# Performance work log

Measured on AMD Instinct MI355X. Metric: run time of the kernel, lower is better.

## Reference

```python
import jax, jax.numpy as jnp
import numpy as np

CAPACITY_FACTOR = 1.25


def setup_inputs() -> dict:
    key = jax.random.key(0)
    ks = jax.random.split(key, 5)
    B, N, D, E, H = 4, 2048, 1024, 8, 4096
    x = jax.random.normal(ks[0], (B, N, D), dtype=jnp.float32)
    w_router = jax.random.normal(ks[1], (D, E), dtype=jnp.float32) * 0.02
    w1 = jax.random.normal(ks[2], (E, D, H), dtype=jnp.float32) * 0.02
    b1 = jnp.zeros((E, H), dtype=jnp.float32)
    w2 = jax.random.normal(ks[3], (E, H, D), dtype=jnp.float32) * 0.02
    b2 = jnp.zeros((E, D), dtype=jnp.float32)
    return {"x": x, "w_router": w_router, "w1": w1, "b1": b1, "w2": w2, "b2": b2}


def reference(x, w_router, w1, b1, w2, b2):
    B, N, D = x.shape
    E = w_router.shape[1]
    C = int(N * CAPACITY_FACTOR // E)  # expert capacity

    # ---- top-1 switch router ----
    logits = jnp.einsum('bnd,de->bne', x, w_router)                 # [B,N,E]
    z = jax.nn.logsumexp(logits, axis=-1)                           # [B,N]
    router_z_loss = jnp.mean(z * z)
    probs = jax.nn.softmax(logits, axis=-1)                         # [B,N,E]
    gate = jnp.max(probs, axis=-1)                                  # [B,N]
    idx = jnp.argmax(probs, axis=-1)                                # [B,N]
    mask = jax.nn.one_hot(idx, E, dtype=x.dtype)                    # [B,N,E]

    # load-balancing aux loss (Switch-Transformer style)
    density = jnp.mean(mask, axis=1)                                # [B,E] fraction routed
    density_proxy = jnp.mean(probs, axis=1)                         # [B,E] mean router prob
    aux_loss = jnp.mean(jnp.sum(density * density_proxy, axis=-1)) * (E * E)

    # position within each expert; drop tokens beyond capacity
    pos = jnp.cumsum(mask, axis=1) - 1.0                            # [B,N,E]
    pos = pos.astype(jnp.int32)
    # one_hot zeros out indices outside [0,C); mask zeros unrouted slots
    dispatch = mask[..., None] * jax.nn.one_hot(pos, C, dtype=x.dtype)  # [B,N,E,C]
    combine = dispatch * gate[:, :, None, None]                     # [B,N,E,C]

    # ---- dense dispatch -> grouped expert FFN -> dense combine ----
    expert_inputs = jnp.einsum('bnd,bnec->becd', x, dispatch)       # [B,E,C,D]
    h = jax.nn.gelu(jnp.einsum('becd,edh->bech', expert_inputs, w1)
                    + b1[None, :, None, :])                          # [B,E,C,H]
    expert_outputs = jnp.einsum('bech,ehd->becd', h, w2) + b2[None, :, None, :]
    output = jnp.einsum('becd,bnec->bnd', expert_outputs, combine)  # [B,N,D]
    return output, aux_loss, router_z_loss
```

## Files before the change

### kernel.cpp

```cpp
#include <hip/hip_runtime.h>
#include <hip/hip_bf16.h>
#include <math.h>

#define B_ 4
#define N_ 2048
#define D_ 1024
#define E_ 8
#define H_ 4096
#define C_ 320
#define M_ (B_*C_)

typedef __attribute__((ext_vector_type(8))) short short8;
typedef __attribute__((ext_vector_type(4))) float floatx4;

__device__ __forceinline__ unsigned short f2bf(float f) {
  unsigned u = __builtin_bit_cast(unsigned, f);
  u += 0x7fffu + ((u >> 16) & 1u);
  return (unsigned short)(u >> 16);
}

__device__ __forceinline__ float gelu_fast(float x) {
  float u = 0.7978845608028654f * (x + 0.044715f * x * x * x);
  float t = 1.f - 2.f / (__expf(2.f * u) + 1.f);
  return 0.5f * x * (1.f + t);
}

__device__ __forceinline__ void gload_lds16(const unsigned short* g, unsigned short* l) {
  __builtin_amdgcn_global_load_lds(
      (const __attribute__((address_space(1))) unsigned int*)g,
      (__attribute__((address_space(3))) unsigned int*)l, 16, 0, 0);
}

__global__ __launch_bounds__(256) void router_kernel(
    const float* __restrict__ x, const float* __restrict__ wr,
    int* __restrict__ idx_buf, float* __restrict__ gate_buf,
    float* __restrict__ stats)
{
  int lane  = threadIdx.x & 63;
  int wave  = threadIdx.x >> 6;
  int token = blockIdx.x * 4 + wave;
  int b     = token >> 11;

  const float* xp = x + (size_t)token * D_ + lane * 16;
  float xv[16];
#pragma unroll
  for (int i = 0; i < 4; i++) {
    float4 v = ((const float4*)xp)[i];
    xv[i*4+0]=v.x; xv[i*4+1]=v.y; xv[i*4+2]=v.z; xv[i*4+3]=v.w;
  }
  double acc[8];
#pragma unroll
  for (int e = 0; e < 8; e++) acc[e] = 0.0;
  const float* wp = wr + (size_t)(lane * 16) * E_;
#pragma unroll
  for (int i = 0; i < 16; i++) {
    float xs = xv[i];
#pragma unroll
    for (int e = 0; e < 8; e++) acc[e] += (double)xs * (double)wp[i*8 + e];
  }
  for (int off = 32; off > 0; off >>= 1) {
#pragma unroll
    for (int e = 0; e < 8; e++) acc[e] += __shfl_xor(acc[e], off, 64);
  }

  float l[8];
#pragma unroll
  for (int e = 0; e < 8; e++) l[e] = (float)acc[e];
  float m = l[0]; int best = 0;
#pragma unroll
  for (int e = 1; e < 8; e++) if (l[e] > m) { m = l[e]; best = e; }
  float p[8], sum = 0.f;
#pragma unroll
  for (int e = 0; e < 8; e++) { p[e] = expf(l[e] - m); sum += p[e]; }
  float inv = 1.f / sum;
#pragma unroll
  for (int e = 0; e < 8; e++) p[e] *= inv;
  float z    = m + logf(sum);
  float gate = inv;

  __shared__ float s_cnt[8], s_prox[8], s_zsq[1];
  if (threadIdx.x < 8)  { s_cnt[threadIdx.x] = 0.f; s_prox[threadIdx.x] = 0.f; }
  if (threadIdx.x == 8) s_zsq[0] = 0.f;
  __syncthreads();
  if (lane == 0) {
    idx_buf[token]  = best;
    gate_buf[token] = gate;
    atomicAdd(&s_zsq[0], z * z);
    atomicAdd(&s_cnt[best], 1.f);
#pragma unroll
    for (int e = 0; e < 8; e++) atomicAdd(&s_prox[e], p[e]);
  }
  __syncthreads();
  if (threadIdx.x < 8) {
    atomicAdd(&stats[b*8 + threadIdx.x],      s_cnt[threadIdx.x]);
    atomicAdd(&stats[32 + b*8 + threadIdx.x], s_prox[threadIdx.x]);
  }
  if (threadIdx.x == 8) atomicAdd(&stats[64], s_zsq[0]);
}

__global__ __launch_bounds__(64) void pos_kernel(
    const int* __restrict__ idx_buf, int* __restrict__ slot_token,
    const float* __restrict__ stats, float* __restrict__ loss_out)
{
  int be = blockIdx.x;
  int b = be >> 3, e = be & 7;
  int lane = threadIdx.x;
  int base = 0;
  int* out = slot_token + (size_t)(e * B_ + b) * C_;
  for (int n0 = 0; n0 < N_; n0 += 64) {
    int n = n0 + lane;
    bool match = (idx_buf[b * N_ + n] == e);
    unsigned long long mask = __ballot(match);
    int my = base + __popcll(mask & ((1ull << lane) - 1ull));
    if (match && my < C_) out[my] = b * N_ + n;
    base += __popcll(mask);
  }
  if (be == 0 && lane == 0) {
    float aux = 0.f;
    for (int i = 0; i < 32; i++) aux += stats[i] * stats[32 + i];
    aux *= 64.f / ((float)B_ * (float)N_ * (float)N_);
    loss_out[0] = aux;
    loss_out[1] = stats[64] / (float)(B_ * N_);
  }
}

__global__ __launch_bounds__(256) void gather_kernel(
    const float* __restrict__ x, const int* __restrict__ slot_token,
    unsigned short* __restrict__ xe)
{
  int row = blockIdx.x;
  int t = slot_token[row];
  int col = threadIdx.x * 4;
  ushort4 o;
  if (t >= 0) {
    float4 v = *(const float4*)(x + (size_t)t * D_ + col);
    o.x = f2bf(v.x); o.y = f2bf(v.y); o.z = f2bf(v.z); o.w = f2bf(v.w);
  } else {
    o.x = 0; o.y = 0; o.z = 0; o.w = 0;
  }
  *(ushort4*)(xe + (size_t)row * D_ + col) = o;
}

__global__ __launch_bounds__(256) void transcast_kernel(
    const float* __restrict__ in, unsigned short* __restrict__ out, int R, int Cc)
{
  int e = blockIdx.z;
  const float* pin = in + (size_t)e * R * Cc;
  unsigned short* pout = out + (size_t)e * R * Cc;
  __shared__ float T[64][65];
  int r0 = blockIdx.y * 64, c0 = blockIdx.x * 64;
  {
    int row = threadIdx.x >> 2;
    int cb  = (threadIdx.x & 3) * 4;
#pragma unroll
    for (int p = 0; p < 4; p++) {
      int col = cb + p * 16;
      float4 v = *(const float4*)(pin + (size_t)(r0 + row) * Cc + c0 + col);
      T[row][col+0] = v.x; T[row][col+1] = v.y; T[row][col+2] = v.z; T[row][col+3] = v.w;
    }
  }
  __syncthreads();
  {
    int ocb = threadIdx.x >> 4;
    int or4 = (threadIdx.x & 15) * 4;
#pragma unroll
    for (int p = 0; p < 4; p++) {
      int oc = ocb + p * 16;
      ushort4 o;
      o.x = f2bf(T[or4+0][oc]); o.y = f2bf(T[or4+1][oc]);
      o.z = f2bf(T[or4+2][oc]); o.w = f2bf(T[or4+3][oc]);
      *(ushort4*)(pout + (size_t)(c0 + oc) * R + r0 + or4) = o;
    }
  }
}

template<int EPI>
__global__ __launch_bounds__(512, 2) void gemm_kernel(
    const unsigned short* __restrict__ A,
    const unsigned short* __restrict__ BT,
    const float* __restrict__ bias,
    unsigned short* __restrict__ Hout,
    float* __restrict__ Out,
    const int* __restrict__ slot_token,
    const float* __restrict__ gate_buf,
    int M, int K, int Nn, int MT)
{
  int e  = blockIdx.x & 7;
  int s  = blockIdx.x >> 3;
  int m0 = (s % MT) * 256;
  int n0 = (s / MT) * 256;
  const unsigned short* Ae = A  + (size_t)e * M  * K;
  const unsigned short* Be = BT + (size_t)e * Nn * K;

  __shared__ __align__(16) unsigned short As[2][256 * 64];
  __shared__ __align__(16) unsigned short Bs[2][256 * 64];
  __shared__ int   s_tok[256];
  __shared__ float s_gate[256];

  int tid  = threadIdx.x;
  int lane = tid & 63;
  int w    = tid >> 6;
  int wm   = (w >> 2) * 128;
  int wn   = (w & 3) * 64;
  int lr   = lane & 15;
  int quad = lane >> 4;
  int c0 = (((quad    ) ^ (lane & 7)) << 3);
  int c1 = (((quad + 4) ^ (lane & 7)) << 3);

  if constexpr (EPI == 1) {
    if (tid < 256) {
      int t = slot_token[(size_t)e * M + m0 + tid];
      s_tok[tid]  = t;
      s_gate[tid] = (t >= 0) ? gate_buf[t] : 0.f;
    }
  }

  floatx4 acc[8][4];
#pragma unroll
  for (int i = 0; i < 8; i++)
#pragma unroll
    for (int j = 0; j < 4; j++) acc[i][j] = (floatx4){0.f, 0.f, 0.f, 0.f};

  int rrow = lane >> 3;
  int sch  = ((lane & 7) ^ rrow) << 3;
  const unsigned short* gA00 = Ae + (size_t)(m0       + w*16     + rrow) * K + sch;
  const unsigned short* gA01 = Ae + (size_t)(m0       + w*16 + 8 + rrow) * K + sch;
  const unsigned short* gA10 = Ae + (size_t)(m0 + 128 + w*16     + rrow) * K + sch;
  const unsigned short* gA11 = Ae + (size_t)(m0 + 128 + w*16 + 8 + rrow) * K + sch;
  const unsigned short* gB00 = Be + (size_t)(n0       + w*16     + rrow) * K + sch;
  const unsigned short* gB01 = Be + (size_t)(n0       + w*16 + 8 + rrow) * K + sch;
  const unsigned short* gB10 = Be + (size_t)(n0 + 128 + w*16     + rrow) * K + sch;
  const unsigned short* gB11 = Be + (size_t)(n0 + 128 + w*16 + 8 + rrow) * K + sch;

#define STAGE_A(dbuf) do { \
    gload_lds16(gA00, &As[dbuf][(w*16    ) * 64]); \
    gload_lds16(gA01, &As[dbuf][(w*16 + 8) * 64]); \
    gload_lds16(gA10, &As[dbuf][(128 + w*16    ) * 64]); \
    gload_lds16(gA11, &As[dbuf][(128 + w*16 + 8) * 64]); \
    gA00 += 64; gA01 += 64; gA10 += 64; gA11 += 64; } while (0)
#define STAGE_B(dbuf) do { \
    gload_lds16(gB00, &Bs[dbuf][(w*16    ) * 64]); \
    gload_lds16(gB01, &Bs[dbuf][(w*16 + 8) * 64]); \
    gload_lds16(gB10, &Bs[dbuf][(128 + w*16    ) * 64]); \
    gload_lds16(gB11, &Bs[dbuf][(128 + w*16 + 8) * 64]); \
    gB00 += 64; gB01 += 64; gB10 += 64; gB11 += 64; } while (0)

  int nt = K >> 6;
  STAGE_A(0); STAGE_B(0);
  if (nt > 1) {
    STAGE_A(1); STAGE_B(1);
    asm volatile("s_waitcnt vmcnt(8)" ::: "memory");
  } else {
    asm volatile("s_waitcnt vmcnt(0)" ::: "memory");
  }
  __builtin_amdgcn_s_barrier();

  short8 af[4][2], bf[4][2];
  int cur = 0;
  for (int t = 0; t < nt; ++t) {
    int nxt = cur ^ 1;
    bool pf = (t + 2 < nt);
#pragma unroll
    for (int m = 0; m < 4; ++m) {
      int row = wm + m * 16 + lr;
      af[m][0] = *(const short8*)&As[cur][row * 64 + c0];
      af[m][1] = *(const short8*)&As[cur][row * 64 + c1];
    }
#pragma unroll
    for (int n = 0; n < 2; ++n) {
      int row = wn + n * 16 + lr;
      bf[n][0] = *(const short8*)&Bs[cur][row * 64 + c0];
      bf[n][1] = *(const short8*)&Bs[cur][row * 64 + c1];
    }
    __builtin_amdgcn_s_barrier();
    asm volatile("s_waitcnt lgkmcnt(0)" ::: "memory");
    __builtin_amdgcn_sched_barrier(0);
    __builtin_amdgcn_s_setprio(1);
#pragma unroll
    for (int m = 0; m < 4; ++m)
#pragma unroll
      for (int n = 0; n < 2; ++n) {
        acc[m][n] = __builtin_amdgcn_mfma_f32_16x16x32_bf16(af[m][0], bf[n][0], acc[m][n], 0, 0, 0);
        acc[m][n] = __builtin_amdgcn_mfma_f32_16x16x32_bf16(af[m][1], bf[n][1], acc[m][n], 0, 0, 0);
      }
    __builtin_amdgcn_s_setprio(0);
    __builtin_amdgcn_s_barrier();
#pragma unroll
    for (int n = 0; n < 2; ++n) {
      int row = wn + (n + 2) * 16 + lr;
      bf[n+2][0] = *(const short8*)&Bs[cur][row * 64 + c0];
      bf[n+2][1] = *(const short8*)&Bs[cur][row * 64 + c1];
    }
    __builtin_amdgcn_s_barrier();
    asm volatile("s_waitcnt lgkmcnt(0)" ::: "memory");
    __builtin_amdgcn_sched_barrier(0);
    __builtin_amdgcn_s_setprio(1);
#pragma unroll
    for (int m = 0; m < 4; ++m)
#pragma unroll
      for (int n = 2; n < 4; ++n) {
        acc[m][n] = __builtin_amdgcn_mfma_f32_16x16x32_bf16(af[m][0], bf[n][0], acc[m][n], 0, 0, 0);
        acc[m][n] = __builtin_amdgcn_mfma_f32_16x16x32_bf16(af[m][1], bf[n][1], acc[m][n], 0, 0, 0);
      }
    __builtin_amdgcn_s_setprio(0);
    __builtin_amdgcn_s_barrier();
#pragma unroll
    for (int m = 0; m < 4; ++m) {
      int row = wm + 64 + m * 16 + lr;
      af[m][0] = *(const short8*)&As[cur][row * 64 + c0];
      af[m][1] = *(const short8*)&As[cur][row * 64 + c1];
    }
    if (pf) STAGE_B(cur);
    __builtin_amdgcn_s_barrier();
    asm volatile("s_waitcnt lgkmcnt(0)" ::: "memory");
    __builtin_amdgcn_sched_barrier(0);
    __builtin_amdgcn_s_setprio(1);
#pragma unroll
    for (int m = 0; m < 4; ++m)
#pragma unroll
      for (int n = 2; n < 4; ++n) {
        acc[m+4][n] = __builtin_amdgcn_mfma_f32_16x16x32_bf16(af[m][0], bf[n][0], acc[m+4][n], 0, 0, 0);
        acc[m+4][n] = __builtin_amdgcn_mfma_f32_16x16x32_bf16(af[m][1], bf[n][1], acc[m+4][n], 0, 0, 0);
      }
    __builtin_amdgcn_s_setprio(0);
    __builtin_amdgcn_s_barrier();
    if (pf) STAGE_A(cur);
    __builtin_amdgcn_s_barrier();
    __builtin_amdgcn_s_setprio(1);
#pragma unroll
    for (int m = 0; m < 4; ++m)
#pragma unroll
      for (int n = 0; n < 2; ++n) {
        acc[m+4][n] = __builtin_amdgcn_mfma_f32_16x16x32_bf16(af[m][0], bf[n][0], acc[m+4][n], 0, 0, 0);
        acc[m+4][n] = __builtin_amdgcn_mfma_f32_16x16x32_bf16(af[m][1], bf[n][1], acc[m+4][n], 0, 0, 0);
      }
    __builtin_amdgcn_s_setprio(0);
    if (pf)                asm volatile("s_waitcnt vmcnt(8)" ::: "memory");
    else if (t + 1 < nt)   asm volatile("s_waitcnt vmcnt(0)" ::: "memory");
    __builtin_amdgcn_s_barrier();
    cur = nxt;
  }
#undef STAGE_A
#undef STAGE_B

#pragma unroll
  for (int m = 0; m < 8; ++m) {
    int rloc = wm + m * 16 + quad * 4;
#pragma unroll
    for (int n = 0; n < 4; ++n) {
      int col = n0 + wn + n * 16 + lr;
      float bz = bias[(size_t)e * Nn + col];
      if constexpr (EPI == 0) {
        size_t base = (size_t)e * M * Nn + (size_t)(m0 + rloc) * Nn + col;
#pragma unroll
        for (int r = 0; r < 4; r++)
          Hout[base + (size_t)r * Nn] = f2bf(gelu_fast(acc[m][n][r] + bz));
      } else {
#pragma unroll
        for (int r = 0; r < 4; r++) {
          int t = s_tok[rloc + r];
          if (t >= 0)
            Out[(size_t)t * D_ + col] = s_gate[rloc + r] * (acc[m][n][r] + bz);
        }
      }
    }
  }
}

extern "C" void kernel_launch(void* const* d_in, const int* in_sizes, int n_in,
                              void* d_out, int out_size, void* d_ws, size_t ws_size,
                              hipStream_t stream)
{
  (void)in_sizes; (void)n_in; (void)ws_size;
  const float* x  = (const float*)d_in[0];
  const float* wr = (const float*)d_in[1];
  const float* w1 = (const float*)d_in[2];
  const float* b1 = (const float*)d_in[3];
  const float* w2 = (const float*)d_in[4];
  const float* b2 = (const float*)d_in[5];
  float* out = (float*)d_out;

  char* ws = (char*)d_ws;
  int*   idx_buf  = (int*)(ws + 0);
  float* gate_buf = (float*)(ws + 32768);
  float* stats    = (float*)(ws + 65536);
  int*   slot_tok = (int*)(ws + 66560);
  unsigned short* xe  = (unsigned short*)(ws + 107520);
  unsigned short* wbf = (unsigned short*)(ws + 21079040);
  unsigned short* hbf = (unsigned short*)(ws + 88187904);

  hipMemsetAsync(d_out, 0, (size_t)out_size * 4, stream);
  hipMemsetAsync(stats, 0, 1024, stream);
  hipMemsetAsync(slot_tok, 0xFF, (size_t)E_ * B_ * C_ * 4, stream);

  router_kernel<<<(B_ * N_) / 4, 256, 0, stream>>>(x, wr, idx_buf, gate_buf, stats);
  pos_kernel<<<B_ * E_, 64, 0, stream>>>(idx_buf, slot_tok, stats,
                                         out + (size_t)B_ * N_ * D_);
  gather_kernel<<<E_ * M_, 256, 0, stream>>>(x, slot_tok, xe);

  transcast_kernel<<<dim3(H_ / 64, D_ / 64, E_), 256, 0, stream>>>(w1, wbf, D_, H_);
  gemm_kernel<0><<<E_ * (H_ / 256) * (M_ / 256), 512, 0, stream>>>(
      xe, wbf, b1, hbf, nullptr, nullptr, nullptr, M_, D_, H_, M_ / 256);
  transcast_kernel<<<dim3(D_ / 64, H_ / 64, E_), 256, 0, stream>>>(w2, wbf, H_, D_);
  gemm_kernel<1><<<E_ * (D_ / 256) * (M_ / 256), 512, 0, stream>>>(
      hbf, wbf, b2, nullptr, out, slot_tok, gate_buf, M_, H_, D_, M_ / 256);
}
```

Baseline: 661.0 us.

## Software-pipeline LDS fragment reads across MFMA phases and cut barriers per k-tile

Restructures the GEMM main loop so LDS fragment reads for the next phase, including the next k-tile's A0/B0, are issued before or during the current MFMA block, using partial lgkmcnt waits instead of full waits. Barriers per iteration drop from about eight to two. Global addressing switches from eight 64-bit pointers to two 32-bit byte offsets to cut scalar and vector register pressure. The risks are higher register use from separate fragment arrays and subtle hazards if the wait counts do not match the number of outstanding loads.

Result: no change. 671.8 us (+1.6%).

```diff
diff --git a/kernel.cpp b/kernel.cpp
--- a/kernel.cpp
+++ b/kernel.cpp
@@ -223,125 +223,124 @@
 
   int rrow = lane >> 3;
   int sch  = ((lane & 7) ^ rrow) << 3;
-  const unsigned short* gA00 = Ae + (size_t)(m0       + w*16     + rrow) * K + sch;
-  const unsigned short* gA01 = Ae + (size_t)(m0       + w*16 + 8 + rrow) * K + sch;
-  const unsigned short* gA10 = Ae + (size_t)(m0 + 128 + w*16     + rrow) * K + sch;
-  const unsigned short* gA11 = Ae + (size_t)(m0 + 128 + w*16 + 8 + rrow) * K + sch;
-  const unsigned short* gB00 = Be + (size_t)(n0       + w*16     + rrow) * K + sch;
-  const unsigned short* gB01 = Be + (size_t)(n0       + w*16 + 8 + rrow) * K + sch;
-  const unsigned short* gB10 = Be + (size_t)(n0 + 128 + w*16     + rrow) * K + sch;
-  const unsigned short* gB11 = Be + (size_t)(n0 + 128 + w*16 + 8 + rrow) * K + sch;
+  unsigned kA   = (unsigned)K * 2;
+  unsigned aoff = (unsigned)(m0 + w*16 + rrow) * kA + (unsigned)sch * 2;
+  unsigned boff = (unsigned)(n0 + w*16 + rrow) * kA + (unsigned)sch * 2;
+  const char* AeC = (const char*)Ae;
+  const char* BeC = (const char*)Be;
 
 #define STAGE_A(dbuf) do { \
-    gload_lds16(gA00, &As[dbuf][(w*16    ) * 64]); \
-    gload_lds16(gA01, &As[dbuf][(w*16 + 8) * 64]); \
-    gload_lds16(gA10, &As[dbuf][(128 + w*16    ) * 64]); \
-    gload_lds16(gA11, &As[dbuf][(128 + w*16 + 8) * 64]); \
-    gA00 += 64; gA01 += 64; gA10 += 64; gA11 += 64; } while (0)
+    gload_lds16((const unsigned short*)(AeC + aoff),            &As[dbuf][(w*16    ) * 64]); \
+    gload_lds16((const unsigned short*)(AeC + aoff +   8*kA),   &As[dbuf][(w*16 + 8) * 64]); \
+    gload_lds16((const unsigned short*)(AeC + aoff + 128*kA),   &As[dbuf][(128 + w*16    ) * 64]); \
+    gload_lds16((const unsigned short*)(AeC + aoff + 136*kA),   &As[dbuf][(128 + w*16 + 8) * 64]); \
+    aoff += 128; } while (0)
 #define STAGE_B(dbuf) do { \
-    gload_lds16(gB00, &Bs[dbuf][(w*16    ) * 64]); \
-    gload_lds16(gB01, &Bs[dbuf][(w*16 + 8) * 64]); \
-    gload_lds16(gB10, &Bs[dbuf][(128 + w*16    ) * 64]); \
-    gload_lds16(gB11, &Bs[dbuf][(128 + w*16 + 8) * 64]); \
-    gB00 += 64; gB01 += 64; gB10 += 64; gB11 += 64; } while (0)
+    gload_lds16((const unsigned short*)(BeC + boff),            &Bs[dbuf][(w*16    ) * 64]); \
+    gload_lds16((const unsigned short*)(BeC + boff +   8*kA),   &Bs[dbuf][(w*16 + 8) * 64]); \
+    gload_lds16((const unsigned short*)(BeC + boff + 128*kA),   &Bs[dbuf][(128 + w*16    ) * 64]); \
+    gload_lds16((const unsigned short*)(BeC + boff + 136*kA),   &Bs[dbuf][(128 + w*16 + 8) * 64]); \
+    boff += 128; } while (0)
+
+  short8 a0[4][2], a1[4][2], b0[2][2], b1[2][2];
+
+#define READ_A0(buf) do { _Pragma("unroll") \
+    for (int m_ = 0; m_ < 4; ++m_) { int row = wm + m_ * 16 + lr; \
+      a0[m_][0] = *(const short8*)&As[buf][row * 64 + c0]; \
+      a0[m_][1] = *(const short8*)&As[buf][row * 64 + c1]; } } while (0)
+#define READ_A1(buf) do { _Pragma("unroll") \
+    for (int m_ = 0; m_ < 4; ++m_) { int row = wm + 64 + m_ * 16 + lr; \
+      a1[m_][0] = *(const short8*)&As[buf][row * 64 + c0]; \
+      a1[m_][1] = *(const short8*)&As[buf][row * 64 + c1]; } } while (0)
+#define READ_B0(buf) do { _Pragma("unroll") \
+    for (int n_ = 0; n_ < 2; ++n_) { int row = wn + n_ * 16 + lr; \
+      b0[n_][0] = *(const short8*)&Bs[buf][row * 64 + c0]; \
+      b0[n_][1] = *(const short8*)&Bs[buf][row * 64 + c1]; } } while (0)
+#define READ_B1(buf) do { _Pragma("unroll") \
+    for (int n_ = 0; n_ < 2; ++n_) { int row = wn + 32 + n_ * 16 + lr; \
+      b1[n_][0] = *(const short8*)&Bs[buf][row * 64 + c0]; \
+      b1[n_][1] = *(const short8*)&Bs[buf][row * 64 + c1]; } } while (0)
+
+#define SB0 __builtin_amdgcn_sched_barrier(0)
 
   int nt = K >> 6;
   STAGE_A(0); STAGE_B(0);
   if (nt > 1) {
-    STAGE_A(1); STAGE_B(1);
+    STAGE_B(1); STAGE_A(1);
     asm volatile("s_waitcnt vmcnt(8)" ::: "memory");
   } else {
     asm volatile("s_waitcnt vmcnt(0)" ::: "memory");
   }
   __builtin_amdgcn_s_barrier();
-
-  short8 af[4][2], bf[4][2];
+  READ_A0(0); READ_B0(0);
+
   int cur = 0;
   for (int t = 0; t < nt; ++t) {
     int nxt = cur ^ 1;
-    bool pf = (t + 2 < nt);
-#pragma unroll
-    for (int m = 0; m < 4; ++m) {
-      int row = wm + m * 16 + lr;
-      af[m][0] = *(const short8*)&As[cur][row * 64 + c0];
-      af[m][1] = *(const short8*)&As[cur][row * 64 + c1];
-    }
-#pragma unroll
-    for (int n = 0; n < 2; ++n) {
-      int row = wn + n * 16 + lr;
-      bf[n][0] = *(const short8*)&Bs[cur][row * 64 + c0];
-      bf[n][1] = *(const short8*)&Bs[cur][row * 64 + c1];
-    }
-    __builtin_amdgcn_s_barrier();
-    asm volatile("s_waitcnt lgkmcnt(0)" ::: "memory");
-    __builtin_amdgcn_sched_barrier(0);
+    READ_B1(cur);
+    SB0;
+    asm volatile("s_waitcnt lgkmcnt(4)" ::: "memory");
+    SB0;
     __builtin_amdgcn_s_setprio(1);
 #pragma unroll
     for (int m = 0; m < 4; ++m)
 #pragma unroll
       for (int n = 0; n < 2; ++n) {
-        acc[m][n] = __builtin_amdgcn_mfma_f32_16x16x32_bf16(af[m][0], bf[n][0], acc[m][n], 0, 0, 0);
-        acc[m][n] = __builtin_amdgcn_mfma_f32_16x16x32_bf16(af[m][1], bf[n][1], acc[m][n], 0, 0, 0);
+        acc[m][n] = __builtin_amdgcn_mfma_f32_16x16x32_bf16(a0[m][0], b0[n][0], acc[m][n], 0, 0, 0);
+        acc[m][n] = __builtin_amdgcn_mfma_f32_16x16x32_bf16(a0[m][1], b0[n][1], acc[m][n], 0, 0, 0);
+      }
+    __builtin_amdgcn_s_setprio(0);
+    READ_A1(cur);
+    SB0;
+    asm volatile("s_waitcnt lgkmcnt(8)" ::: "memory");
+    SB0;
+    __builtin_amdgcn_s_setprio(1);
+#pragma unroll
+    for (int m = 0; m < 4; ++m)
+#pragma unroll
+      for (int n = 0; n < 2; ++n) {
+        acc[m][n+2] = __builtin_amdgcn_mfma_f32_16x16x32_bf16(a0[m][0], b1[n][0], acc[m][n+2], 0, 0, 0);
+        acc[m][n+2] = __builtin_amdgcn_mfma_f32_16x16x32_bf16(a0[m][1], b1[n][1], acc[m][n+2], 0, 0, 0);
       }
     __builtin_amdgcn_s_setprio(0);
     __builtin_amdgcn_s_barrier();
-#pragma unroll
-    for (int n = 0; n < 2; ++n) {
-      int row = wn + (n + 2) * 16 + lr;
-      bf[n+2][0] = *(const short8*)&Bs[cur][row * 64 + c0];
-      bf[n+2][1] = *(const short8*)&Bs[cur][row * 64 + c1];
-    }
-    __builtin_amdgcn_s_barrier();
+    if (t + 2 < nt) STAGE_B(cur);
+    SB0;
     asm volatile("s_waitcnt lgkmcnt(0)" ::: "memory");
-    __builtin_amdgcn_sched_barrier(0);
+    SB0;
     __builtin_amdgcn_s_setprio(1);
 #pragma unroll
     for (int m = 0; m < 4; ++m)
 #pragma unroll
-      for (int n = 2; n < 4; ++n) {
-        acc[m][n] = __builtin_amdgcn_mfma_f32_16x16x32_bf16(af[m][0], bf[n][0], acc[m][n], 0, 0, 0);
-        acc[m][n] = __builtin_amdgcn_mfma_f32_16x16x32_bf16(af[m][1], bf[n][1], acc[m][n], 0, 0, 0);
+      for (int n = 0; n < 2; ++n) {
+        acc[m+4][n] = __builtin_amdgcn_mfma_f32_16x16x32_bf16(a1[m][0], b0[n][0], acc[m+4][n], 0, 0, 0);
+        acc[m+4][n] = __builtin_amdgcn_mfma_f32_16x16x32_bf16(a1[m][1], b0[n][1], acc[m+4][n], 0, 0, 0);
       }
     __builtin_amdgcn_s_setprio(0);
+    if (t + 2 < nt)      asm volatile("s_waitcnt vmcnt(4)" ::: "memory");
+    else if (t + 1 < nt) asm volatile("s_waitcnt vmcnt(0)" ::: "memory");
     __builtin_amdgcn_s_barrier();
-#pragma unroll
-    for (int m = 0; m < 4; ++m) {
-      int row = wm + 64 + m * 16 + lr;
-      af[m][0] = *(const short8*)&As[cur][row * 64 + c0];
-      af[m][1] = *(const short8*)&As[cur][row * 64 + c1];
-    }
-    if (pf) STAGE_B(cur);
-    __builtin_amdgcn_s_barrier();
-    asm volatile("s_waitcnt lgkmcnt(0)" ::: "memory");
-    __builtin_amdgcn_sched_barrier(0);
+    if (t + 2 < nt) STAGE_A(cur);
+    if (t + 1 < nt) { READ_A0(nxt); READ_B0(nxt); }
+    SB0;
     __builtin_amdgcn_s_setprio(1);
 #pragma unroll
     for (int m = 0; m < 4; ++m)
 #pragma unroll
-      for (int n = 2; n < 4; ++n) {
-        acc[m+4][n] = __builtin_amdgcn_mfma_f32_16x16x32_bf16(af[m][0], bf[n][0], acc[m+4][n], 0, 0, 0);
-        acc[m+4][n] = __builtin_amdgcn_mfma_f32_16x16x32_bf16(af[m][1], bf[n][1], acc[m+4][n], 0, 0, 0);
+      for (int n = 0; n < 2; ++n) {
+        acc[m+4][n+2] = __builtin_amdgcn_mfma_f32_16x16x32_bf16(a1[m][0], b1[n][0], acc[m+4][n+2], 0, 0, 0);
+        acc[m+4][n+2] = __builtin_amdgcn_mfma_f32_16x16x32_bf16(a1[m][1], b1[n][1], acc[m+4][n+2], 0, 0, 0);
       }
     __builtin_amdgcn_s_setprio(0);
-    __builtin_amdgcn_s_barrier();
-    if (pf) STAGE_A(cur);
-    __builtin_amdgcn_s_barrier();
-    __builtin_amdgcn_s_setprio(1);
-#pragma unroll
-    for (int m = 0; m < 4; ++m)
-#pragma unroll
-      for (int n = 0; n < 2; ++n) {
-        acc[m+4][n] = __builtin_amdgcn_mfma_f32_16x16x32_bf16(af[m][0], bf[n][0], acc[m+4][n], 0, 0, 0);
-        acc[m+4][n] = __builtin_amdgcn_mfma_f32_16x16x32_bf16(af[m][1], bf[n][1], acc[m+4][n], 0, 0, 0);
-      }
-    __builtin_amdgcn_s_setprio(0);
-    if (pf)                asm volatile("s_waitcnt vmcnt(8)" ::: "memory");
-    else if (t + 1 < nt)   asm volatile("s_waitcnt vmcnt(0)" ::: "memory");
-    __builtin_amdgcn_s_barrier();
     cur = nxt;
   }
 #undef STAGE_A
 #undef STAGE_B
+#undef READ_A0
+#undef READ_A1
+#undef READ_B0
+#undef READ_B1
+#undef SB0
 
 #pragma unroll
   for (int m = 0; m < 8; ++m) {
```
